# Optimization experiments

Measured on AMD Instinct MI355X. Metric: run time of the kernel, lower is better.

## Reference

```python
import jax, jax.numpy as jnp
import numpy as np

B, TIN, NB, H, SOUT, R, G = 64, 49, 24, 384, 10, 2, 5  # batch, in_frames, bones, hidden, out_frames, rec_steps, gates(i,fs,ft,o,c)


def setup_inputs() -> dict:
    key = jax.random.key(0)
    ks = jax.random.split(key, 9)
    s = 1.0 / np.sqrt(H)  # scaled init so gates don't saturate (original uses randn)
    return {
        "hidden_states": jax.random.normal(ks[0], (B, TIN, NB, H), jnp.float32),
        "cell_states": jax.random.normal(ks[1], (B, TIN, NB, H), jnp.float32),
        "global_t_state": jax.random.normal(ks[2], (B, NB, H), jnp.float32),
        "global_s_state": jax.random.normal(ks[3], (B, TIN, H), jnp.float32),
        "p": jax.random.normal(ks[4], (B, SOUT, NB, H), jnp.float32),
        # per (rec_step, bone) cell weights: x / h_temporal / h_spatial projections for 5 gates
        "U": jax.random.normal(ks[5], (R, NB, G, H, H), jnp.float32) * s,
        "Wt": jax.random.normal(ks[6], (R, NB, G, H, H), jnp.float32) * s,
        "Ws": jax.random.normal(ks[7], (R, NB, G, H, H), jnp.float32) * s,
        "b": jax.random.normal(ks[8], (R, NB, G, H), jnp.float32) * s,
    }


def _cell(Ub, Wtb, Wsb, bb, x, ht, hs, ct, cs):
    # Ub/Wtb/Wsb: [G,H,H], bb: [G,H]; x/ht/hs/ct/cs: [B,H]
    g = (jnp.einsum('bh,ghk->bgk', x, Ub)
         + jnp.einsum('bh,ghk->bgk', ht, Wtb)
         + jnp.einsum('bh,ghk->bgk', hs, Wsb) + bb)
    i_n = jax.nn.sigmoid(g[:, 0])
    f_s = jax.nn.sigmoid(g[:, 1])
    f_t = jax.nn.sigmoid(g[:, 2])
    o_n = jax.nn.sigmoid(g[:, 3])
    c_n = jnp.tanh(g[:, 4])
    c_h = i_n * c_n + f_t * ct + f_s * cs
    return o_n * jnp.tanh(c_h), c_h


def reference(hidden_states, cell_states, global_t_state, global_s_state, p, U, Wt, Ws, b):
    # rec step 0: h_t = h_s = hidden_states; rec step 1: h_t = cat(global_t, hidden), h_s = hidden
    h_t1 = jnp.concatenate([global_t_state[:, None], hidden_states], axis=1)
    hm = hidden_states.mean(axis=(1, 2))                    # [B,H] spatial boundary (bone 0) for both steps
    cm = cell_states.mean(axis=(1, 2))
    bound_h = jnp.stack([hm, hm])                            # [R,B,H]
    bound_c = jnp.stack([cm, cm])
    h_prev = jnp.stack([hidden_states.mean(1), h_t1.mean(1)])  # [R,B,NB,H] frame-0 row (bones 1:)
    c_prev = jnp.stack([cell_states.mean(1)] * 2)

    Un, Wtn, Wsn, bn = (jnp.swapaxes(a, 0, 1) for a in (U, Wt, Ws, b))  # [NB,R,...]

    def frame_step(carry, p_f):  # p_f: [NB,B,H]
        h_prev, c_prev = carry                              # [R,B,NB,H]
        hp_n = jnp.moveaxis(h_prev, 2, 0)                   # [NB,R,B,H]
        cp_n = jnp.moveaxis(c_prev, 2, 0)

        def bone_step(bc, xs):
            hl, cl = bc                                     # [R,B,H] left-neighbor (spatial) state
            Ub, Wtb, Wsb, bb, x0, hp, cp = xs
            h0, c0 = _cell(Ub[0], Wtb[0], Wsb[0], bb[0], x0, hp[0], hl[0], cp[0], cl[0])
            h1, c1 = _cell(Ub[1], Wtb[1], Wsb[1], bb[1], h0, hp[1], hl[1], cp[1], cl[1])
            hn = jnp.stack([h0, h1])
            cn = jnp.stack([c0, c1])
            return (hn, cn), (hn, cn)

        _, (hs_all, cs_all) = jax.lax.scan(
            bone_step, (bound_h, bound_c), (Un, Wtn, Wsn, bn, p_f, hp_n, cp_n))
        h_new = jnp.moveaxis(hs_all, 0, 2)                  # [R,B,NB,H]
        c_new = jnp.moveaxis(cs_all, 0, 2)
        return (h_new, c_new), (h_new[-1], c_new[-1])

    p_frames = jnp.transpose(p, (1, 2, 0, 3))               # [SOUT,NB,B,H]
    _, (h_out, c_out) = jax.lax.scan(frame_step, (h_prev, c_prev), p_frames)
    return jnp.moveaxis(h_out, 0, 1), jnp.moveaxis(c_out, 0, 1)  # [B,SOUT,NB,H] each
```

## Files before the change

### kernel.cpp

```cpp
#include <hip/hip_runtime.h>

#define BATCH 64
#define TIN   49
#define NB    24
#define HID   384
#define SOUT  10
#define NGATE 5

typedef __attribute__((ext_vector_type(4))) float f32x4;
typedef __attribute__((ext_vector_type(8))) short short8v;

__device__ __forceinline__ unsigned short f2bf(float f) {
    union { float f; unsigned u; } v; v.f = f;
    unsigned r = v.u + 0x7fffu + ((v.u >> 16) & 1u);
    return (unsigned short)(r >> 16);
}
__device__ __forceinline__ float bf2f(unsigned short h) {
    union { unsigned u; float f; } v; v.u = ((unsigned)h) << 16; return v.f;
}

#define NW2_BLK 25920
#define NP_BLK  23040
#define NM_BLK  576

__global__ __launch_bounds__(256) void prologue_kernel(
    const float* __restrict__ U, const float* __restrict__ Wt,
    const float* __restrict__ Ws, const float* __restrict__ p,
    const float* __restrict__ hid, const float* __restrict__ cel,
    const float* __restrict__ gt,
    unsigned short* __restrict__ wpack, unsigned short* __restrict__ pb,
    unsigned short* __restrict__ hp_b, float* __restrict__ cp_f)
{
    __shared__ unsigned short tile[64][68];
    int bx = blockIdx.x;
    if (bx < NW2_BLK) {
        int q = bx;
        int cb = q % 6; q /= 6;
        int kb = q % 6; q /= 6;
        int m  = q % 3; q /= 3;
        int g  = q % 5; q /= 5;
        int cell = q;
        const float* W = (m == 0) ? U : (m == 1) ? Wt : Ws;
        const float* src = W + ((size_t)(cell * NGATE + g) * HID + kb * 64) * HID + cb * 64;
        int t = threadIdx.x;
        int kr = t >> 4, c4 = (t & 15) * 4;
#pragma unroll
        for (int i = 0; i < 4; ++i) {
            float4 v = *(const float4*)(src + (size_t)(kr + 16 * i) * HID + c4);
            tile[kr + 16 * i][c4 + 0] = f2bf(v.x);
            tile[kr + 16 * i][c4 + 1] = f2bf(v.y);
            tile[kr + 16 * i][c4 + 2] = f2bf(v.z);
            tile[kr + 16 * i][c4 + 3] = f2bf(v.w);
        }
        __syncthreads();
#pragma unroll
        for (int ii = 0; ii < 2; ++ii) {
            int e = t + 256 * ii;
            int lane = e & 63; int qq = e >> 6;
            int pair = qq & 1, kc2 = (qq >> 1) & 1, t2 = qq >> 2;
            int kl = kc2 * 32 + (lane >> 4) * 8;
            int cl = t2 * 32 + pair * 16 + (lane & 15);
            unsigned short o[8];
#pragma unroll
            for (int jj = 0; jj < 8; ++jj) o[jj] = tile[kl + jj][cl];
            int t32 = cb * 2 + t2;
            int kc  = m * 12 + kb * 2 + kc2;
            size_t dst = ((size_t)((cell * 12 + t32) * NGATE + g) * (36 * 2)
                          + kc * 2 + pair) * 64 + lane;
            *(short8v*)(wpack + dst * 8) = *(const short8v*)o;
        }
    } else if (bx < NW2_BLK + NP_BLK) {
        size_t idx = (size_t)(bx - NW2_BLK) * 256 + threadIdx.x;
        int h = (int)(idx % HID);
        size_t q = idx / HID;
        int b = (int)(q % BATCH); q /= BATCH;
        int n = (int)(q % NB); q /= NB;
        int f = (int)q;
        pb[idx] = f2bf(p[((size_t)(b * SOUT + f) * NB + n) * HID + h]);
    } else {
        int idx = (bx - NW2_BLK - NP_BLK) * 256 + threadIdx.x;
        const int total4 = NB * BATCH * HID / 4;
        if (idx >= total4) return;
        const int H4 = HID / 4;
        int h = (idx % H4) * 4;
        int b = (idx / H4) % BATCH;
        int n = idx / (H4 * BATCH);
        const int fs4 = NB * HID / 4;
        const float4* ph = (const float4*)(hid + ((size_t)b * TIN * NB + n) * HID + h);
        const float4* pc = (const float4*)(cel + ((size_t)b * TIN * NB + n) * HID + h);
        float sh[4] = {0,0,0,0}, sc[4] = {0,0,0,0};
        for (int t = 0; t < TIN; ++t) {
            float4 vh = ph[(size_t)t * fs4];
            float4 vc = pc[(size_t)t * fs4];
            sh[0] += vh.x; sh[1] += vh.y; sh[2] += vh.z; sh[3] += vh.w;
            sc[0] += vc.x; sc[1] += vc.y; sc[2] += vc.z; sc[3] += vc.w;
        }
        float4 g4 = *(const float4*)(gt + ((size_t)b * NB + n) * HID + h);
        const float* g_ = (const float*)&g4;
        unsigned short o0[4], o1[4];
        float c0[4];
#pragma unroll
        for (int j = 0; j < 4; ++j) {
            o0[j] = f2bf(sh[j] / TIN);
            o1[j] = f2bf((g_[j] + sh[j]) / (TIN + 1));
            c0[j] = sc[j] / TIN;
        }
        size_t base = (size_t)idx * 4;
        const size_t tot = (size_t)NB * BATCH * HID;
        *(uint2*)(hp_b + base)       = *(const uint2*)o0;
        *(uint2*)(hp_b + tot + base) = *(const uint2*)o1;
        *(float4*)(cp_f + base)       = make_float4(c0[0], c0[1], c0[2], c0[3]);
        *(float4*)(cp_f + tot + base) = make_float4(c0[0], c0[1], c0[2], c0[3]);
    }
}

__global__ void init_bounds_kernel(const unsigned short* __restrict__ hp_b,
                                   const float* __restrict__ cp_f,
                                   unsigned short* __restrict__ bh_b,
                                   float* __restrict__ bc_f) {
    int idx = blockIdx.x * blockDim.x + threadIdx.x;
    if (idx >= BATCH * HID) return;
    float sh = 0.f, sc = 0.f;
    for (int n = 0; n < NB; ++n) {
        sh += bf2f(hp_b[(size_t)n * BATCH * HID + idx]);
        sc += cp_f[(size_t)n * BATCH * HID + idx];
    }
    bh_b[idx] = f2bf(sh / NB);
    bc_f[idx] = sc / NB;
}

union SMem {
    unsigned short A[2][64][392];
    float gl[2][NGATE][64][35];
};

__global__ __launch_bounds__(640) void cell_fused_kernel(
    int d, int A0,
    const unsigned short* __restrict__ pb,
    const unsigned short* __restrict__ wpack,
    const float* __restrict__ bias,
    const unsigned short* __restrict__ hp_b,
    const float* __restrict__ cp_f,
    const unsigned short* __restrict__ bh_b,
    const float* __restrict__ bc_f,
    unsigned short* __restrict__ h_sl,
    float* __restrict__ c_sl,
    float* __restrict__ out)
{
    __shared__ SMem sm;

    int y = blockIdx.y;
    int rstep, dg;
    if (y < A0) { rstep = 0; dg = d; }
    else        { rstep = 1; dg = d - 1; y -= A0; }
    int lo = dg - (SOUT - 1); if (lo < 0) lo = 0;
    const int n = lo + y;
    const int f = dg - n;
    const int cur = dg & 1, prv = cur ^ 1;
    const int t = blockIdx.x;
    const int wv   = threadIdx.x >> 6;
    const int gate = wv % NGATE;
    const int kh   = wv / NGATE;
    const int lane = threadIdx.x & 63;
    const int S = BATCH * HID;
    const int cell = rstep * NB + n;

    const unsigned short *xb, *htb, *hsb;
    const float *ctb, *csb;
    if (rstep == 0) {
        xb  = pb + (size_t)(f * NB + n) * S;
        htb = f ? h_sl + (size_t)((prv * 2 + 0) * NB + n) * S : hp_b + (size_t)n * S;
        hsb = n ? h_sl + (size_t)((prv * 2 + 0) * NB + n - 1) * S : bh_b;
        ctb = f ? c_sl + (size_t)((prv * 2 + 0) * NB + n) * S : cp_f + (size_t)n * S;
        csb = n ? c_sl + (size_t)((prv * 2 + 0) * NB + n - 1) * S : bc_f;
    } else {
        xb  = h_sl + (size_t)((cur * 2 + 0) * NB + n) * S;
        htb = f ? h_sl + (size_t)((prv * 2 + 1) * NB + n) * S
                : hp_b + (size_t)(NB + n) * S;
        hsb = n ? h_sl + (size_t)((prv * 2 + 1) * NB + n - 1) * S : bh_b;
        ctb = f ? c_sl + (size_t)((prv * 2 + 1) * NB + n) * S
                : cp_f + (size_t)(NB + n) * S;
        csb = n ? c_sl + (size_t)((prv * 2 + 1) * NB + n - 1) * S : bc_f;
    }

    const int eb = threadIdx.x & 63;
    const int ecq = (threadIdx.x >> 6) & 3;
    float4 cth[2], csh[2];
    if (threadIdx.x < 256) {
#pragma unroll
        for (int h = 0; h < 2; ++h) {
            int colg = t * 32 + h * 16 + ecq * 4;
            cth[h] = *(const float4*)(ctb + (size_t)eb * HID + colg);
            csh[h] = *(const float4*)(csb + (size_t)eb * HID + colg);
        }
    }

    uint4 streg[5];
    auto STAGE_LOAD = [&](const unsigned short* src) {
#pragma unroll
        for (int i = 0; i < 5; ++i) {
            int c = (int)threadIdx.x + i * 640;
            if (i < 4 || c < 3072) {
                int row = c / 48, cc = c - row * 48;
                streg[i] = *(const uint4*)(src + (size_t)row * HID + cc * 8);
            }
        }
    };
    auto STAGE_WRITE = [&](int buf) {
#pragma unroll
        for (int i = 0; i < 5; ++i) {
            int c = (int)threadIdx.x + i * 640;
            if (i < 4 || c < 3072) {
                int row = c / 48, cc = c - row * 48;
                *(uint4*)&sm.A[buf][row][cc * 8] = streg[i];
            }
        }
    };

    const short8v* wp = (const short8v*)wpack
        + (size_t)((cell * 12 + t) * NGATE + gate) * (36 * 2 * 64);

    f32x4 acc[2][4];
#pragma unroll
    for (int pr = 0; pr < 2; ++pr)
#pragma unroll
        for (int q = 0; q < 4; ++q) acc[pr][q] = (f32x4){0, 0, 0, 0};

    const int arow = lane & 15;
    const int akg  = (lane >> 4) * 8;

    auto COMPUTE = [&](int m, int buf) {
        const short8v* wbm = wp + (size_t)((m * 12 + kh * 6) * 2) * 64 + lane;
        short8v bufB[3][2];
#pragma unroll
        for (int j = 0; j < 3; ++j) {
            bufB[j][0] = wbm[(size_t)j * 128];
            bufB[j][1] = wbm[(size_t)j * 128 + 64];
        }
#pragma unroll
        for (int j = 0; j < 6; ++j) {
            const int koff = kh * 192 + j * 32 + akg;
            short8v a[4];
#pragma unroll
            for (int q = 0; q < 4; ++q)
                a[q] = *(const short8v*)&sm.A[buf][arow + q * 16][koff];
            const int sl = j % 3;
#pragma unroll
            for (int q = 0; q < 4; ++q) {
                acc[0][q] = __builtin_amdgcn_mfma_f32_16x16x32_bf16(a[q], bufB[sl][0], acc[0][q], 0, 0, 0);
                acc[1][q] = __builtin_amdgcn_mfma_f32_16x16x32_bf16(a[q], bufB[sl][1], acc[1][q], 0, 0, 0);
            }
            if (j < 3) {
                bufB[sl][0] = wbm[(size_t)(j + 3) * 128];
                bufB[sl][1] = wbm[(size_t)(j + 3) * 128 + 64];
            }
        }
    };

    STAGE_LOAD(xb);
    STAGE_WRITE(0);
    __syncthreads();

    STAGE_LOAD(htb);
    COMPUTE(0, 0);
    __syncthreads();
    STAGE_WRITE(1);
    __syncthreads();

    STAGE_LOAD(hsb);
    COMPUTE(1, 1);
    __syncthreads();
    STAGE_WRITE(0);
    __syncthreads();

    COMPUTE(2, 0);
    __syncthreads();

#pragma unroll
    for (int pr = 0; pr < 2; ++pr)
#pragma unroll
        for (int q = 0; q < 4; ++q)
#pragma unroll
            for (int i = 0; i < 4; ++i)
                sm.gl[kh][gate][q * 16 + (lane >> 4) * 4 + i][pr * 16 + (lane & 15)]
                    = acc[pr][q][i];
    __syncthreads();

    if (threadIdx.x < 256) {
        size_t dbase = (size_t)((cur * 2 + rstep) * NB + n) * S + (size_t)eb * HID;
        const float* bbase = bias + (size_t)cell * NGATE * HID;
#pragma unroll
        for (int h = 0; h < 2; ++h) {
            int cloc = h * 16 + ecq * 4;
            int colg = t * 32 + cloc;
            const float* ct_ = (const float*)&cth[h];
            const float* cs_ = (const float*)&csh[h];
            float hv4[4], ch4[4];
            unsigned short hb4[4];
#pragma unroll
            for (int cc = 0; cc < 4; ++cc) {
                float gi  = sm.gl[0][0][eb][cloc + cc] + sm.gl[1][0][eb][cloc + cc] + bbase[0 * HID + colg + cc];
                float gfs = sm.gl[0][1][eb][cloc + cc] + sm.gl[1][1][eb][cloc + cc] + bbase[1 * HID + colg + cc];
                float gft = sm.gl[0][2][eb][cloc + cc] + sm.gl[1][2][eb][cloc + cc] + bbase[2 * HID + colg + cc];
                float go  = sm.gl[0][3][eb][cloc + cc] + sm.gl[1][3][eb][cloc + cc] + bbase[3 * HID + colg + cc];
                float gc  = sm.gl[0][4][eb][cloc + cc] + sm.gl[1][4][eb][cloc + cc] + bbase[4 * HID + colg + cc];
                float i_n = 1.f / (1.f + __expf(-gi));
                float f_s = 1.f / (1.f + __expf(-gfs));
                float f_t = 1.f / (1.f + __expf(-gft));
                float o_n = 1.f / (1.f + __expf(-go));
                float c_n = tanhf(gc);
                float ch  = i_n * c_n + f_t * ct_[cc] + f_s * cs_[cc];
                float hv  = o_n * tanhf(ch);
                hv4[cc] = hv; ch4[cc] = ch; hb4[cc] = f2bf(hv);
            }
            *(uint2*)(h_sl + dbase + colg) = *(const uint2*)hb4;
            *(float4*)(c_sl + dbase + colg) = make_float4(ch4[0], ch4[1], ch4[2], ch4[3]);
            if (rstep == 1) {
                size_t o = ((size_t)(eb * SOUT + f) * NB + n) * HID + colg;
                *(float4*)(out + o) = make_float4(hv4[0], hv4[1], hv4[2], hv4[3]);
                *(float4*)(out + (size_t)BATCH * SOUT * NB * HID + o)
                    = make_float4(ch4[0], ch4[1], ch4[2], ch4[3]);
            }
        }
    }
}

extern "C" void kernel_launch(void* const* d_in, const int* in_sizes, int n_in,
                              void* d_out, int out_size, void* d_ws, size_t ws_size,
                              hipStream_t stream) {
    const float* hid  = (const float*)d_in[0];
    const float* cel  = (const float*)d_in[1];
    const float* gt   = (const float*)d_in[2];
    const float* p    = (const float*)d_in[4];
    const float* U    = (const float*)d_in[5];
    const float* Wt   = (const float*)d_in[6];
    const float* Ws   = (const float*)d_in[7];
    const float* bias = (const float*)d_in[8];
    float* out = (float*)d_out;

    char* cur_ = (char*)d_ws;
    auto carve = [&](size_t bytes) -> void* {
        void* r = cur_; cur_ += (bytes + 255) & ~(size_t)255; return r;
    };
    const size_t NPBH = (size_t)NB * BATCH * HID;
    unsigned short* wpack = (unsigned short*)carve((size_t)13271040 * 16);
    unsigned short* pb    = (unsigned short*)carve((size_t)SOUT * NB * BATCH * HID * 2);
    unsigned short* hp_b  = (unsigned short*)carve(2 * NPBH * 2);
    float*          cp_f  = (float*)carve(2 * NPBH * 4);
    unsigned short* bh_b  = (unsigned short*)carve((size_t)BATCH * HID * 2);
    float*          bc_f  = (float*)carve((size_t)BATCH * HID * 4);
    unsigned short* h_sl  = (unsigned short*)carve(4 * NPBH * 2);
    float*          c_sl  = (float*)carve(4 * NPBH * 4);

    prologue_kernel<<<NW2_BLK + NP_BLK + NM_BLK, 256, 0, stream>>>(
        U, Wt, Ws, p, hid, cel, gt, wpack, pb, hp_b, cp_f);
    init_bounds_kernel<<<(BATCH * HID + 255) / 256, 256, 0, stream>>>(
        hp_b, cp_f, bh_b, bc_f);

    auto cnt = [](int dg) {
        int lo = dg - (SOUT - 1); if (lo < 0) lo = 0;
        int hi = (dg < NB - 1) ? dg : NB - 1;
        return hi - lo + 1;
    };
    for (int d = 0; d < SOUT + NB; ++d) {
        int A0 = (d <= SOUT + NB - 2) ? cnt(d) : 0;
        int A1 = (d >= 1) ? cnt(d - 1) : 0;
        dim3 grid(12, A0 + A1);
        cell_fused_kernel<<<grid, 640, 0, stream>>>(d, A0, pb, wpack, bias,
                                                    hp_b, cp_f, bh_b, bc_f,
                                                    h_sl, c_sl, out);
    }
}
```

Before: 1.268 ms.

## Replace per-diagonal launches with persistent dataflow kernel using atomic ticket scheduling

The 34 wavefront-diagonal kernel launches are replaced by one persistent kernel of 256 workgroups. Each workgroup grabs work items through an atomic ticket counter and spin-waits on per-cell done counters for its temporal, spatial and rec-step dependencies. This lets tiles start as soon as their inputs are ready instead of waiting at launch boundaries. Each item also prefetches its weight tile before waiting, and the split-K partial sums are reduced in place in shared memory to shrink LDS use. The state buffers grow to hold every (cell, frame) result, and correctness relies on ticket ordering to avoid deadlock among resident workgroups.

```diff
diff --git a/kernel.cpp b/kernel.cpp
--- a/kernel.cpp
+++ b/kernel.cpp
@@ -22,6 +22,8 @@
 #define NW2_BLK 25920
 #define NP_BLK  23040
 #define NM_BLK  576
+#define NITEMS  5760
+#define PGRID   256
 
 __global__ __launch_bounds__(256) void prologue_kernel(
     const float* __restrict__ U, const float* __restrict__ Wt,
@@ -129,13 +131,13 @@
     bc_f[idx] = sc / NB;
 }
 
-union SMem {
-    unsigned short A[2][64][392];
-    float gl[2][NGATE][64][35];
-};
-
-__global__ __launch_bounds__(640) void cell_fused_kernel(
-    int d, int A0,
+__global__ void reset_kernel(int* done, int* tick) {
+    int i = blockIdx.x * blockDim.x + threadIdx.x;
+    if (i < 2 * NB * SOUT) done[i] = 0;
+    if (i == 0) *tick = 0;
+}
+
+__global__ __launch_bounds__(640) void persist_kernel(
     const unsigned short* __restrict__ pb,
     const unsigned short* __restrict__ wpack,
     const float* __restrict__ bias,
@@ -143,185 +145,259 @@
     const float* __restrict__ cp_f,
     const unsigned short* __restrict__ bh_b,
     const float* __restrict__ bc_f,
-    unsigned short* __restrict__ h_sl,
-    float* __restrict__ c_sl,
-    float* __restrict__ out)
+    unsigned short* __restrict__ h_st,
+    float* __restrict__ c_st,
+    float* __restrict__ out,
+    int* __restrict__ done,
+    int* __restrict__ tick)
 {
-    __shared__ SMem sm;
-
-    int y = blockIdx.y;
-    int rstep, dg;
-    if (y < A0) { rstep = 0; dg = d; }
-    else        { rstep = 1; dg = d - 1; y -= A0; }
-    int lo = dg - (SOUT - 1); if (lo < 0) lo = 0;
-    const int n = lo + y;
-    const int f = dg - n;
-    const int cur = dg & 1, prv = cur ^ 1;
-    const int t = blockIdx.x;
     const int wv   = threadIdx.x >> 6;
     const int gate = wv % NGATE;
     const int kh   = wv / NGATE;
     const int lane = threadIdx.x & 63;
     const int S = BATCH * HID;
-    const int cell = rstep * NB + n;
-
-    const unsigned short *xb, *htb, *hsb;
-    const float *ctb, *csb;
-    if (rstep == 0) {
-        xb  = pb + (size_t)(f * NB + n) * S;
-        htb = f ? h_sl + (size_t)((prv * 2 + 0) * NB + n) * S : hp_b + (size_t)n * S;
-        hsb = n ? h_sl + (size_t)((prv * 2 + 0) * NB + n - 1) * S : bh_b;
-        ctb = f ? c_sl + (size_t)((prv * 2 + 0) * NB + n) * S : cp_f + (size_t)n * S;
-        csb = n ? c_sl + (size_t)((prv * 2 + 0) * NB + n - 1) * S : bc_f;
-    } else {
-        xb  = h_sl + (size_t)((cur * 2 + 0) * NB + n) * S;
-        htb = f ? h_sl + (size_t)((prv * 2 + 1) * NB + n) * S
-                : hp_b + (size_t)(NB + n) * S;
-        hsb = n ? h_sl + (size_t)((prv * 2 + 1) * NB + n - 1) * S : bh_b;
-        ctb = f ? c_sl + (size_t)((prv * 2 + 1) * NB + n) * S
-                : cp_f + (size_t)(NB + n) * S;
-        csb = n ? c_sl + (size_t)((prv * 2 + 1) * NB + n - 1) * S : bc_f;
-    }
-
-    const int eb = threadIdx.x & 63;
-    const int ecq = (threadIdx.x >> 6) & 3;
-    float4 cth[2], csh[2];
-    if (threadIdx.x < 256) {
-#pragma unroll
-        for (int h = 0; h < 2; ++h) {
-            int colg = t * 32 + h * 16 + ecq * 4;
-            cth[h] = *(const float4*)(ctb + (size_t)eb * HID + colg);
-            csh[h] = *(const float4*)(csb + (size_t)eb * HID + colg);
-        }
-    }
-
-    uint4 streg[5];
-    auto STAGE_LOAD = [&](const unsigned short* src) {
-#pragma unroll
-        for (int i = 0; i < 5; ++i) {
-            int c = (int)threadIdx.x + i * 640;
-            if (i < 4 || c < 3072) {
-                int row = c / 48, cc = c - row * 48;
-                streg[i] = *(const uint4*)(src + (size_t)row * HID + cc * 8);
-            }
-        }
-    };
-    auto STAGE_WRITE = [&](int buf) {
-#pragma unroll
-        for (int i = 0; i < 5; ++i) {
-            int c = (int)threadIdx.x + i * 640;
-            if (i < 4 || c < 3072) {
-                int row = c / 48, cc = c - row * 48;
-                *(uint4*)&sm.A[buf][row][cc * 8] = streg[i];
-            }
-        }
-    };
-
-    const short8v* wp = (const short8v*)wpack
-        + (size_t)((cell * 12 + t) * NGATE + gate) * (36 * 2 * 64);
-
-    f32x4 acc[2][4];
-#pragma unroll
-    for (int pr = 0; pr < 2; ++pr)
-#pragma unroll
-        for (int q = 0; q < 4; ++q) acc[pr][q] = (f32x4){0, 0, 0, 0};
-
-    const int arow = lane & 15;
-    const int akg  = (lane >> 4) * 8;
-
-    auto COMPUTE = [&](int m, int buf) {
-        const short8v* wbm = wp + (size_t)((m * 12 + kh * 6) * 2) * 64 + lane;
-        short8v bufB[3][2];
-#pragma unroll
-        for (int j = 0; j < 3; ++j) {
-            bufB[j][0] = wbm[(size_t)j * 128];
-            bufB[j][1] = wbm[(size_t)j * 128 + 64];
-        }
-#pragma unroll
-        for (int j = 0; j < 6; ++j) {
-            const int koff = kh * 192 + j * 32 + akg;
-            short8v a[4];
-#pragma unroll
-            for (int q = 0; q < 4; ++q)
-                a[q] = *(const short8v*)&sm.A[buf][arow + q * 16][koff];
-            const int sl = j % 3;
-#pragma unroll
-            for (int q = 0; q < 4; ++q) {
-                acc[0][q] = __builtin_amdgcn_mfma_f32_16x16x32_bf16(a[q], bufB[sl][0], acc[0][q], 0, 0, 0);
-                acc[1][q] = __builtin_amdgcn_mfma_f32_16x16x32_bf16(a[q], bufB[sl][1], acc[1][q], 0, 0, 0);
-            }
-            if (j < 3) {
-                bufB[sl][0] = wbm[(size_t)(j + 3) * 128];
-                bufB[sl][1] = wbm[(size_t)(j + 3) * 128 + 64];
-            }
-        }
-    };
-
-    STAGE_LOAD(xb);
-    STAGE_WRITE(0);
-    __syncthreads();
-
-    STAGE_LOAD(htb);
-    COMPUTE(0, 0);
-    __syncthreads();
-    STAGE_WRITE(1);
-    __syncthreads();
-
-    STAGE_LOAD(hsb);
-    COMPUTE(1, 1);
-    __syncthreads();
-    STAGE_WRITE(0);
-    __syncthreads();
-
-    COMPUTE(2, 0);
-    __syncthreads();
-
-#pragma unroll
-    for (int pr = 0; pr < 2; ++pr)
-#pragma unroll
-        for (int q = 0; q < 4; ++q)
-#pragma unroll
-            for (int i = 0; i < 4; ++i)
-                sm.gl[kh][gate][q * 16 + (lane >> 4) * 4 + i][pr * 16 + (lane & 15)]
-                    = acc[pr][q][i];
-    __syncthreads();
-
-    if (threadIdx.x < 256) {
-        size_t dbase = (size_t)((cur * 2 + rstep) * NB + n) * S + (size_t)eb * HID;
-        const float* bbase = bias + (size_t)cell * NGATE * HID;
-#pragma unroll
-        for (int h = 0; h < 2; ++h) {
-            int cloc = h * 16 + ecq * 4;
-            int colg = t * 32 + cloc;
-            const float* ct_ = (const float*)&cth[h];
-            const float* cs_ = (const float*)&csh[h];
-            float hv4[4], ch4[4];
-            unsigned short hb4[4];
-#pragma unroll
-            for (int cc = 0; cc < 4; ++cc) {
-                float gi  = sm.gl[0][0][eb][cloc + cc] + sm.gl[1][0][eb][cloc + cc] + bbase[0 * HID + colg + cc];
-                float gfs = sm.gl[0][1][eb][cloc + cc] + sm.gl[1][1][eb][cloc + cc] + bbase[1 * HID + colg + cc];
-                float gft = sm.gl[0][2][eb][cloc + cc] + sm.gl[1][2][eb][cloc + cc] + bbase[2 * HID + colg + cc];
-                float go  = sm.gl[0][3][eb][cloc + cc] + sm.gl[1][3][eb][cloc + cc] + bbase[3 * HID + colg + cc];
-                float gc  = sm.gl[0][4][eb][cloc + cc] + sm.gl[1][4][eb][cloc + cc] + bbase[4 * HID + colg + cc];
-                float i_n = 1.f / (1.f + __expf(-gi));
-                float f_s = 1.f / (1.f + __expf(-gfs));
-                float f_t = 1.f / (1.f + __expf(-gft));
-                float o_n = 1.f / (1.f + __expf(-go));
-                float c_n = tanhf(gc);
-                float ch  = i_n * c_n + f_t * ct_[cc] + f_s * cs_[cc];
-                float hv  = o_n * tanhf(ch);
-                hv4[cc] = hv; ch4[cc] = ch; hb4[cc] = f2bf(hv);
-            }
-            *(uint2*)(h_sl + dbase + colg) = *(const uint2*)hb4;
-            *(float4*)(c_sl + dbase + colg) = make_float4(ch4[0], ch4[1], ch4[2], ch4[3]);
-            if (rstep == 1) {
-                size_t o = ((size_t)(eb * SOUT + f) * NB + n) * HID + colg;
-                *(float4*)(out + o) = make_float4(hv4[0], hv4[1], hv4[2], hv4[3]);
-                *(float4*)(out + (size_t)BATCH * SOUT * NB * HID + o)
-                    = make_float4(ch4[0], ch4[1], ch4[2], ch4[3]);
-            }
-        }
+
+    __shared__ unsigned short Ab[2][64][392];
+    __shared__ float gl[NGATE][64][35];
+    __shared__ int s_tkt;
+
+    for (;;) {
+        __syncthreads();
+        if (threadIdx.x == 0)
+            s_tkt = __hip_atomic_fetch_add(tick, 1, __ATOMIC_RELAXED,
+                                           __HIP_MEMORY_SCOPE_AGENT);
+        __syncthreads();
+        const int T = s_tkt;
+        if (T >= NITEMS) return;
+
+        int rem = T, r = 0, lo = 0, d = 0;
+        for (int s = 0;; ++s) {
+            d = s >> 1; r = s & 1;
+            lo = d - (SOUT - 1); if (lo < 0) lo = 0;
+            int hi = (d < NB - 1) ? d : NB - 1;
+            int c = (hi - lo + 1) * 12;
+            if (rem < c) break;
+            rem -= c;
+        }
+        const int n = lo + rem / 12;
+        const int t = rem % 12;
+        const int f = d - n;
+        const int cell = r * NB + n;
+        const int ci = cell * SOUT + f;
+
+        const short8v* wp = (const short8v*)wpack
+            + (size_t)((cell * 12 + t) * NGATE + gate) * (36 * 2 * 64);
+
+        {
+            const uint4* wt = (const uint4*)(wp + (size_t)(kh * 6 * 2) * 64 + lane);
+            unsigned dx = 0, dy = 0, dz = 0, dw = 0;
+#pragma unroll
+            for (int s = 0; s < 36; ++s) {
+                int m = s / 12, j = s % 12;
+                uint4 v = wt[((size_t)m * 24 + j) * 64];
+                dx ^= v.x; dy ^= v.y; dz ^= v.z; dw ^= v.w;
+            }
+            asm volatile("" :: "v"(dx), "v"(dy), "v"(dz), "v"(dw) : "memory");
+        }
+
+        {
+            int dep0 = -1, dep1 = -1, dep2 = -1;
+            if (r == 0) {
+                if (f > 0) dep0 = n * SOUT + f - 1;
+                if (n > 0) dep1 = (n - 1) * SOUT + f;
+            } else {
+                dep0 = n * SOUT + f;
+                if (f > 0) dep1 = (NB + n) * SOUT + f - 1;
+                if (n > 0) dep2 = (NB + n - 1) * SOUT + f;
+            }
+            if (threadIdx.x == 0) {
+                int deps[3] = { dep0, dep1, dep2 };
+#pragma unroll
+                for (int i = 0; i < 3; ++i) {
+                    int dp = deps[i];
+                    if (dp < 0) continue;
+                    while (__hip_atomic_load(done + dp, __ATOMIC_RELAXED,
+                                             __HIP_MEMORY_SCOPE_AGENT) < 12)
+                        __builtin_amdgcn_s_sleep(8);
+                    int z = __hip_atomic_load(done + dp, __ATOMIC_ACQUIRE,
+                                              __HIP_MEMORY_SCOPE_AGENT);
+                    asm volatile("" :: "v"(z));
+                }
+            }
+            __syncthreads();
+        }
+
+        const unsigned short *xb, *htb, *hsb;
+        const float *ctb, *csb;
+        if (r == 0) {
+            xb  = pb + (size_t)(f * NB + n) * S;
+            htb = f ? h_st + (size_t)(n * SOUT + f - 1) * S : hp_b + (size_t)n * S;
+            hsb = n ? h_st + (size_t)((n - 1) * SOUT + f) * S : bh_b;
+            ctb = f ? c_st + (size_t)(n * SOUT + f - 1) * S : cp_f + (size_t)n * S;
+            csb = n ? c_st + (size_t)((n - 1) * SOUT + f) * S : bc_f;
+        } else {
+            xb  = h_st + (size_t)(n * SOUT + f) * S;
+            htb = f ? h_st + (size_t)((NB + n) * SOUT + f - 1) * S
+                    : hp_b + (size_t)(NB + n) * S;
+            hsb = n ? h_st + (size_t)((NB + n - 1) * SOUT + f) * S : bh_b;
+            ctb = f ? c_st + (size_t)((NB + n) * SOUT + f - 1) * S
+                    : cp_f + (size_t)(NB + n) * S;
+            csb = n ? c_st + (size_t)((NB + n - 1) * SOUT + f) * S : bc_f;
+        }
+
+        const int eb = threadIdx.x & 63;
+        const int ecq = (threadIdx.x >> 6) & 3;
+        float4 cth[2], csh[2];
+        if (threadIdx.x < 256) {
+#pragma unroll
+            for (int h = 0; h < 2; ++h) {
+                int colg = t * 32 + h * 16 + ecq * 4;
+                cth[h] = *(const float4*)(ctb + (size_t)eb * HID + colg);
+                csh[h] = *(const float4*)(csb + (size_t)eb * HID + colg);
+            }
+        }
+
+        uint4 streg[5];
+        auto STAGE_LOAD = [&](const unsigned short* src) {
+#pragma unroll
+            for (int i = 0; i < 5; ++i) {
+                int c = (int)threadIdx.x + i * 640;
+                if (i < 4 || c < 3072) {
+                    int row = c / 48, cc = c - row * 48;
+                    streg[i] = *(const uint4*)(src + (size_t)row * HID + cc * 8);
+                }
+            }
+        };
+        auto STAGE_WRITE = [&](int buf) {
+#pragma unroll
+            for (int i = 0; i < 5; ++i) {
+                int c = (int)threadIdx.x + i * 640;
+                if (i < 4 || c < 3072) {
+                    int row = c / 48, cc = c - row * 48;
+                    *(uint4*)&Ab[buf][row][cc * 8] = streg[i];
+                }
+            }
+        };
+
+        f32x4 acc[2][4];
+#pragma unroll
+        for (int pr = 0; pr < 2; ++pr)
+#pragma unroll
+            for (int q = 0; q < 4; ++q) acc[pr][q] = (f32x4){0, 0, 0, 0};
+
+        const int arow = lane & 15;
+        const int akg  = (lane >> 4) * 8;
+
+        auto COMPUTE = [&](int m, int buf) {
+            const short8v* wbm = wp + (size_t)((m * 12 + kh * 6) * 2) * 64 + lane;
+            short8v bufB[3][2];
+#pragma unroll
+            for (int j = 0; j < 3; ++j) {
+                bufB[j][0] = wbm[(size_t)j * 128];
+                bufB[j][1] = wbm[(size_t)j * 128 + 64];
+            }
+#pragma unroll
+            for (int j = 0; j < 6; ++j) {
+                const int koff = kh * 192 + j * 32 + akg;
+                short8v a[4];
+#pragma unroll
+                for (int q = 0; q < 4; ++q)
+                    a[q] = *(const short8v*)&Ab[buf][arow + q * 16][koff];
+                const int sl = j % 3;
+#pragma unroll
+                for (int q = 0; q < 4; ++q) {
+                    acc[0][q] = __builtin_amdgcn_mfma_f32_16x16x32_bf16(a[q], bufB[sl][0], acc[0][q], 0, 0, 0);
+                    acc[1][q] = __builtin_amdgcn_mfma_f32_16x16x32_bf16(a[q], bufB[sl][1], acc[1][q], 0, 0, 0);
+                }
+                if (j < 3) {
+                    bufB[sl][0] = wbm[(size_t)(j + 3) * 128];
+                    bufB[sl][1] = wbm[(size_t)(j + 3) * 128 + 64];
+                }
+            }
+        };
+
+        STAGE_LOAD(xb);
+        STAGE_WRITE(0);
+        __syncthreads();
+
+        STAGE_LOAD(htb);
+        COMPUTE(0, 0);
+        __syncthreads();
+        STAGE_WRITE(1);
+        __syncthreads();
+
+        STAGE_LOAD(hsb);
+        COMPUTE(1, 1);
+        __syncthreads();
+        STAGE_WRITE(0);
+        __syncthreads();
+
+        COMPUTE(2, 0);
+
+        if (kh == 1) {
+#pragma unroll
+            for (int pr = 0; pr < 2; ++pr)
+#pragma unroll
+                for (int q = 0; q < 4; ++q)
+#pragma unroll
+                    for (int i = 0; i < 4; ++i)
+                        gl[gate][q * 16 + (lane >> 4) * 4 + i][pr * 16 + (lane & 15)]
+                            = acc[pr][q][i];
+        }
+        __syncthreads();
+        if (kh == 0) {
+#pragma unroll
+            for (int pr = 0; pr < 2; ++pr)
+#pragma unroll
+                for (int q = 0; q < 4; ++q)
+#pragma unroll
+                    for (int i = 0; i < 4; ++i)
+                        gl[gate][q * 16 + (lane >> 4) * 4 + i][pr * 16 + (lane & 15)]
+                            += acc[pr][q][i];
+        }
+        __syncthreads();
+
+        if (threadIdx.x < 256) {
+            size_t dbase = (size_t)ci * S + (size_t)eb * HID;
+            const float* bbase = bias + (size_t)cell * NGATE * HID;
+#pragma unroll
+            for (int h = 0; h < 2; ++h) {
+                int cloc = h * 16 + ecq * 4;
+                int colg = t * 32 + cloc;
+                const float* ct_ = (const float*)&cth[h];
+                const float* cs_ = (const float*)&csh[h];
+                float hv4[4], ch4[4];
+                unsigned short hb4[4];
+#pragma unroll
+                for (int cc = 0; cc < 4; ++cc) {
+                    float gi  = gl[0][eb][cloc + cc] + bbase[0 * HID + colg + cc];
+                    float gfs = gl[1][eb][cloc + cc] + bbase[1 * HID + colg + cc];
+                    float gft = gl[2][eb][cloc + cc] + bbase[2 * HID + colg + cc];
+                    float go  = gl[3][eb][cloc + cc] + bbase[3 * HID + colg + cc];
+                    float gc  = gl[4][eb][cloc + cc] + bbase[4 * HID + colg + cc];
+                    float i_n = 1.f / (1.f + __expf(-gi));
+                    float f_s = 1.f / (1.f + __expf(-gfs));
+                    float f_t = 1.f / (1.f + __expf(-gft));
+                    float o_n = 1.f / (1.f + __expf(-go));
+                    float c_n = tanhf(gc);
+                    float ch  = i_n * c_n + f_t * ct_[cc] + f_s * cs_[cc];
+                    float hv  = o_n * tanhf(ch);
+                    hv4[cc] = hv; ch4[cc] = ch; hb4[cc] = f2bf(hv);
+                }
+                *(uint2*)(h_st + dbase + colg) = *(const uint2*)hb4;
+                *(float4*)(c_st + dbase + colg) = make_float4(ch4[0], ch4[1], ch4[2], ch4[3]);
+                if (r == 1) {
+                    size_t o = ((size_t)(eb * SOUT + f) * NB + n) * HID + colg;
+                    *(float4*)(out + o) = make_float4(hv4[0], hv4[1], hv4[2], hv4[3]);
+                    *(float4*)(out + (size_t)BATCH * SOUT * NB * HID + o)
+                        = make_float4(ch4[0], ch4[1], ch4[2], ch4[3]);
+                }
+            }
+        }
+        __syncthreads();
+        if (threadIdx.x == 0)
+            __hip_atomic_fetch_add(done + ci, 1, __ATOMIC_RELEASE,
+                                   __HIP_MEMORY_SCOPE_AGENT);
     }
 }
 
@@ -349,25 +425,17 @@
     float*          cp_f  = (float*)carve(2 * NPBH * 4);
     unsigned short* bh_b  = (unsigned short*)carve((size_t)BATCH * HID * 2);
     float*          bc_f  = (float*)carve((size_t)BATCH * HID * 4);
-    unsigned short* h_sl  = (unsigned short*)carve(4 * NPBH * 2);
-    float*          c_sl  = (float*)carve(4 * NPBH * 4);
-
+    unsigned short* h_st  = (unsigned short*)carve((size_t)2 * NB * SOUT * BATCH * HID * 2);
+    float*          c_st  = (float*)carve((size_t)2 * NB * SOUT * BATCH * HID * 4);
+    int*            done  = (int*)carve(2 * NB * SOUT * sizeof(int));
+    int*            tick  = (int*)carve(256);
+
+    reset_kernel<<<2, 256, 0, stream>>>(done, tick);
     prologue_kernel<<<NW2_BLK + NP_BLK + NM_BLK, 256, 0, stream>>>(
         U, Wt, Ws, p, hid, cel, gt, wpack, pb, hp_b, cp_f);
     init_bounds_kernel<<<(BATCH * HID + 255) / 256, 256, 0, stream>>>(
         hp_b, cp_f, bh_b, bc_f);
-
-    auto cnt = [](int dg) {
-        int lo = dg - (SOUT - 1); if (lo < 0) lo = 0;
-        int hi = (dg < NB - 1) ? dg : NB - 1;
-        return hi - lo + 1;
-    };
-    for (int d = 0; d < SOUT + NB; ++d) {
-        int A0 = (d <= SOUT + NB - 2) ? cnt(d) : 0;
-        int A1 = (d >= 1) ? cnt(d - 1) : 0;
-        dim3 grid(12, A0 + A1);
-        cell_fused_kernel<<<grid, 640, 0, stream>>>(d, A0, pb, wpack, bias,
-                                                    hp_b, cp_f, bh_b, bc_f,
-                                                    h_sl, c_sl, out);
-    }
-}
+    persist_kernel<<<PGRID, 640, 0, stream>>>(
+        pb, wpack, bias, hp_b, cp_f, bh_b, bc_f,
+        h_st, c_st, out, done, tick);
+}
```

After: 1.569 ms. +23.7%, slower.

## Prefetch full weight matrix slices into registers one stage ahead; widen prologue packing tiles

Applied to the files above, without the earlier changes.

The cell kernel now loads all twelve B-fragments for a weight matrix into registers before the previous matrix's MFMA stage runs. It double-buffers them across the x, h_t and h_s stages, replacing the intra-stage 3-slot rolling prefetch, so global weight latency is hidden behind compute. The prologue weight-pack kernel now converts whole 64x384 row blocks per workgroup instead of 64x64 tiles. That cuts its block count sixfold and uses a larger LDS tile. Holding 24 extra vector registers per thread may raise register pressure and lower occupancy.

```diff
diff --git a/kernel.cpp b/kernel.cpp
--- a/kernel.cpp
+++ b/kernel.cpp
@@ -19,7 +19,7 @@
     union { unsigned u; float f; } v; v.u = ((unsigned)h) << 16; return v.f;
 }
 
-#define NW2_BLK 25920
+#define NW3_BLK 4320
 #define NP_BLK  23040
 #define NM_BLK  576
 
@@ -31,46 +31,45 @@
     unsigned short* __restrict__ wpack, unsigned short* __restrict__ pb,
     unsigned short* __restrict__ hp_b, float* __restrict__ cp_f)
 {
-    __shared__ unsigned short tile[64][68];
+    __shared__ unsigned short tile[64][390];
     int bx = blockIdx.x;
-    if (bx < NW2_BLK) {
+    if (bx < NW3_BLK) {
         int q = bx;
-        int cb = q % 6; q /= 6;
         int kb = q % 6; q /= 6;
         int m  = q % 3; q /= 3;
         int g  = q % 5; q /= 5;
         int cell = q;
         const float* W = (m == 0) ? U : (m == 1) ? Wt : Ws;
-        const float* src = W + ((size_t)(cell * NGATE + g) * HID + kb * 64) * HID + cb * 64;
-        int t = threadIdx.x;
-        int kr = t >> 4, c4 = (t & 15) * 4;
-#pragma unroll
-        for (int i = 0; i < 4; ++i) {
-            float4 v = *(const float4*)(src + (size_t)(kr + 16 * i) * HID + c4);
-            tile[kr + 16 * i][c4 + 0] = f2bf(v.x);
-            tile[kr + 16 * i][c4 + 1] = f2bf(v.y);
-            tile[kr + 16 * i][c4 + 2] = f2bf(v.z);
-            tile[kr + 16 * i][c4 + 3] = f2bf(v.w);
+        const float* src = W + ((size_t)(cell * NGATE + g) * HID + kb * 64) * HID;
+        int tid = threadIdx.x;
+#pragma unroll
+        for (int i = 0; i < 24; ++i) {
+            int c = tid + i * 256;
+            int row = c / 96, c4 = (c % 96) * 4;
+            float4 v = *(const float4*)(src + (size_t)row * HID + c4);
+            tile[row][c4 + 0] = f2bf(v.x);
+            tile[row][c4 + 1] = f2bf(v.y);
+            tile[row][c4 + 2] = f2bf(v.z);
+            tile[row][c4 + 3] = f2bf(v.w);
         }
         __syncthreads();
-#pragma unroll
-        for (int ii = 0; ii < 2; ++ii) {
-            int e = t + 256 * ii;
-            int lane = e & 63; int qq = e >> 6;
-            int pair = qq & 1, kc2 = (qq >> 1) & 1, t2 = qq >> 2;
+        int lane = tid & 63, grp = tid >> 6;
+#pragma unroll
+        for (int uu = 0; uu < 12; ++uu) {
+            int unit = grp * 12 + uu;
+            int pair = unit & 1, kc2 = (unit >> 1) & 1, t32 = unit >> 2;
             int kl = kc2 * 32 + (lane >> 4) * 8;
-            int cl = t2 * 32 + pair * 16 + (lane & 15);
+            int cl = t32 * 32 + pair * 16 + (lane & 15);
             unsigned short o[8];
 #pragma unroll
             for (int jj = 0; jj < 8; ++jj) o[jj] = tile[kl + jj][cl];
-            int t32 = cb * 2 + t2;
-            int kc  = m * 12 + kb * 2 + kc2;
-            size_t dst = ((size_t)((cell * 12 + t32) * NGATE + g) * (36 * 2)
+            int kc = m * 12 + kb * 2 + kc2;
+            size_t dst = ((size_t)((cell * 12 + t32) * NGATE + g) * 72
                           + kc * 2 + pair) * 64 + lane;
             *(short8v*)(wpack + dst * 8) = *(const short8v*)o;
         }
-    } else if (bx < NW2_BLK + NP_BLK) {
-        size_t idx = (size_t)(bx - NW2_BLK) * 256 + threadIdx.x;
+    } else if (bx < NW3_BLK + NP_BLK) {
+        size_t idx = (size_t)(bx - NW3_BLK) * 256 + threadIdx.x;
         int h = (int)(idx % HID);
         size_t q = idx / HID;
         int b = (int)(q % BATCH); q /= BATCH;
@@ -78,7 +77,7 @@
         int f = (int)q;
         pb[idx] = f2bf(p[((size_t)(b * SOUT + f) * NB + n) * HID + h]);
     } else {
-        int idx = (bx - NW2_BLK - NP_BLK) * 256 + threadIdx.x;
+        int idx = (bx - NW3_BLK - NP_BLK) * 256 + threadIdx.x;
         const int total4 = NB * BATCH * HID / 4;
         if (idx >= total4) return;
         const int H4 = HID / 4;
@@ -183,6 +182,18 @@
         csb = n ? c_sl + (size_t)((prv * 2 + 1) * NB + n - 1) * S : bc_f;
     }
 
+    const short8v* wp = (const short8v*)wpack
+        + (size_t)((cell * 12 + t) * NGATE + gate) * (36 * 2 * 64);
+
+    short8v Ba[12], Bb[12];
+    auto LOADB = [&](short8v* B, int m) {
+#pragma unroll
+        for (int u = 0; u < 12; ++u) {
+            int j = u >> 1, pair = u & 1;
+            B[u] = wp[(size_t)(((m * 12 + kh * 6 + j) * 2) + pair) * 64 + lane];
+        }
+    };
+
     const int eb = threadIdx.x & 63;
     const int ecq = (threadIdx.x >> 6) & 3;
     float4 cth[2], csh[2];
@@ -217,9 +228,6 @@
         }
     };
 
-    const short8v* wp = (const short8v*)wpack
-        + (size_t)((cell * 12 + t) * NGATE + gate) * (36 * 2 * 64);
-
     f32x4 acc[2][4];
 #pragma unroll
     for (int pr = 0; pr < 2; ++pr)
@@ -229,14 +237,7 @@
     const int arow = lane & 15;
     const int akg  = (lane >> 4) * 8;
 
-    auto COMPUTE = [&](int m, int buf) {
-        const short8v* wbm = wp + (size_t)((m * 12 + kh * 6) * 2) * 64 + lane;
-        short8v bufB[3][2];
-#pragma unroll
-        for (int j = 0; j < 3; ++j) {
-            bufB[j][0] = wbm[(size_t)j * 128];
-            bufB[j][1] = wbm[(size_t)j * 128 + 64];
-        }
+    auto COMPUTE = [&](int buf, const short8v* B) {
 #pragma unroll
         for (int j = 0; j < 6; ++j) {
             const int koff = kh * 192 + j * 32 + akg;
@@ -244,36 +245,34 @@
 #pragma unroll
             for (int q = 0; q < 4; ++q)
                 a[q] = *(const short8v*)&sm.A[buf][arow + q * 16][koff];
-            const int sl = j % 3;
 #pragma unroll
             for (int q = 0; q < 4; ++q) {
-                acc[0][q] = __builtin_amdgcn_mfma_f32_16x16x32_bf16(a[q], bufB[sl][0], acc[0][q], 0, 0, 0);
-                acc[1][q] = __builtin_amdgcn_mfma_f32_16x16x32_bf16(a[q], bufB[sl][1], acc[1][q], 0, 0, 0);
-            }
-            if (j < 3) {
-                bufB[sl][0] = wbm[(size_t)(j + 3) * 128];
-                bufB[sl][1] = wbm[(size_t)(j + 3) * 128 + 64];
-            }
-        }
-    };
-
+                acc[0][q] = __builtin_amdgcn_mfma_f32_16x16x32_bf16(a[q], B[2 * j],     acc[0][q], 0, 0, 0);
+                acc[1][q] = __builtin_amdgcn_mfma_f32_16x16x32_bf16(a[q], B[2 * j + 1], acc[1][q], 0, 0, 0);
+            }
+        }
+    };
+
+    LOADB(Ba, 0);
     STAGE_LOAD(xb);
     STAGE_WRITE(0);
     __syncthreads();
 
     STAGE_LOAD(htb);
-    COMPUTE(0, 0);
+    LOADB(Bb, 1);
+    COMPUTE(0, Ba);
     __syncthreads();
     STAGE_WRITE(1);
     __syncthreads();
 
     STAGE_LOAD(hsb);
-    COMPUTE(1, 1);
+    LOADB(Ba, 2);
+    COMPUTE(1, Bb);
     __syncthreads();
     STAGE_WRITE(0);
     __syncthreads();
 
-    COMPUTE(2, 0);
+    COMPUTE(0, Ba);
     __syncthreads();
 
 #pragma unroll
@@ -352,7 +351,7 @@
     unsigned short* h_sl  = (unsigned short*)carve(4 * NPBH * 2);
     float*          c_sl  = (float*)carve(4 * NPBH * 4);
 
-    prologue_kernel<<<NW2_BLK + NP_BLK + NM_BLK, 256, 0, stream>>>(
+    prologue_kernel<<<NW3_BLK + NP_BLK + NM_BLK, 256, 0, stream>>>(
         U, Wt, Ws, p, hid, cel, gt, wpack, pb, hp_b, cp_f);
     init_bounds_kernel<<<(BATCH * HID + 255) / 256, 256, 0, stream>>>(
         hp_b, cp_f, bh_b, bc_f);
```

Measured after the change: 1.587 ms. 1.25x slower.
